# Optimization experiments

Measured on AMD Instinct MI355X. Metric: run time of the kernel, lower is better.

## Reference

```python
import jax, jax.numpy as jnp
import numpy as np

N_R, N_V, D, E_RR, L, G = 50000, 2000, 128, 800000, 3, 32


def setup_inputs() -> dict:
    key = jax.random.key(0)
    ks = jax.random.split(key, 10)
    x_real = jax.random.normal(ks[0], (N_R, D), dtype=jnp.float32)
    x_virtual = jax.random.normal(ks[1], (N_V, D), dtype=jnp.float32)
    # params: [num_layers, 3 relations (r_to_r, r_to_v, v_to_r), D, D]
    W_root = jax.random.normal(ks[2], (L, 3, D, D), dtype=jnp.float32) * 0.05
    W_nbr = jax.random.normal(ks[3], (L, 3, D, D), dtype=jnp.float32) * 0.05
    bias = jax.random.normal(ks[4], (L, 3, D), dtype=jnp.float32) * 0.05
    edge_rr = jax.random.randint(ks[5], (2, E_RR), 0, N_R)
    # one virtual-node edge per real node (hierarchical virtual nodes)
    src_rv = jnp.arange(N_R)
    dst_rv = jax.random.randint(ks[6], (N_R,), 0, N_V)
    edge_rv = jnp.stack([src_rv, dst_rv])          # real -> virtual
    edge_vr = jnp.stack([dst_rv, src_rv])          # virtual -> real
    batch_real = jnp.sort(jax.random.randint(ks[7], (N_R,), 0, G))
    return {
        "x_real": x_real, "x_virtual": x_virtual,
        "W_root": W_root, "W_nbr": W_nbr, "bias": bias,
        "edge_rr": edge_rr, "edge_rv": edge_rv, "edge_vr": edge_vr,
        "batch_real": batch_real,
    }


def _graph_conv(x_src, x_dst, src, dst, Wr, Wn, b, n_dst):
    # PyG GraphConv-style: root transform + sum-aggregated neighbor messages
    msg = jax.ops.segment_sum(x_src[src] @ Wn, dst, num_segments=n_dst)
    return x_dst @ Wr + msg + b


def _forward(x_real, x_virtual, W_root, W_nbr, bias, edge_rr, edge_rv, edge_vr, batch_real):
    x_r, x_v = x_real, x_virtual
    n_r, n_v = x_r.shape[0], x_v.shape[0]
    for l in range(W_root.shape[0]):
        # HeteroConv with aggr='sum': sum relation outputs per destination type
        c_rr = _graph_conv(x_r, x_r, edge_rr[0], edge_rr[1], W_root[l, 0], W_nbr[l, 0], bias[l, 0], n_r)
        c_vr = _graph_conv(x_v, x_r, edge_vr[0], edge_vr[1], W_root[l, 2], W_nbr[l, 2], bias[l, 2], n_r)
        c_rv = _graph_conv(x_r, x_v, edge_rv[0], edge_rv[1], W_root[l, 1], W_nbr[l, 1], bias[l, 1], n_v)
        # activation + dropout (eval mode -> identity)
        x_r = jax.nn.relu(c_rr + c_vr)
        x_v = jax.nn.relu(c_rv)
    # mean readout over real nodes per graph
    counts = jax.ops.segment_sum(jnp.ones((n_r,), x_r.dtype), batch_real, num_segments=G)
    graph_emb = jax.ops.segment_sum(x_r, batch_real, num_segments=G) / jnp.maximum(counts, 1.0)[:, None]
    return x_r, graph_emb


def reference(x_real, x_virtual, W_root, W_nbr, bias, edge_rr, edge_rv, edge_vr, batch_real):
    node_embedding, graph_embedding = _forward(
        x_real, x_virtual, W_root, W_nbr, bias, edge_rr, edge_rv, edge_vr, batch_real)
    return node_embedding, graph_embedding
```

## Files before the change

kernel.cpp:

```cpp
#include <hip/hip_runtime.h>
#include <hip/hip_bf16.h>

#define N_R   50000
#define N_V   2000
#define DIM   128
#define E_RR  800000
#define NLAY  3
#define NGR   32
#define RCHUNK 16

#define BUKD  128
#define NBUK  391
#define CHKE  2048
#define NCHK  391

typedef __attribute__((ext_vector_type(8))) short bf16x8;
typedef __attribute__((ext_vector_type(4))) float f32x4;
typedef __attribute__((ext_vector_type(2))) float f32x2;
typedef __attribute__((ext_vector_type(8))) unsigned char u8x8;

__device__ __forceinline__ ushort f2bf(float f) {
    unsigned u = __builtin_bit_cast(unsigned, f);
    unsigned r = (u + 0x7fffu + ((u >> 16) & 1u)) >> 16;
    return (ushort)r;
}
__device__ __forceinline__ float bf2f(ushort h) {
    unsigned u = ((unsigned)h) << 16;
    return __builtin_bit_cast(float, u);
}
__device__ __forceinline__ int lbound(const int* __restrict__ a, int n, int key) {
    int lo = 0, hi = n;
    while (lo < hi) { int mid = (lo + hi) >> 1; if (a[mid] < key) lo = mid + 1; else hi = mid; }
    return lo;
}

__device__ __forceinline__ void acc_u8row(
    unsigned w0, unsigned w1, float s,
    f32x2& a01, f32x2& a23, f32x2& a45, f32x2& a67)
{
    f32x2 sc = {s, s};
    a01 += sc * (f32x2){(float)(w0 & 0xffu), (float)((w0 >> 8) & 0xffu)};
    a23 += sc * (f32x2){(float)((w0 >> 16) & 0xffu), (float)(w0 >> 24)};
    a45 += sc * (f32x2){(float)(w1 & 0xffu), (float)((w1 >> 8) & 0xffu)};
    a67 += sc * (f32x2){(float)((w1 >> 16) & 0xffu), (float)(w1 >> 24)};
}

__global__ __launch_bounds__(256) void hist_kernel(
    const int* __restrict__ dst, int n, int* __restrict__ cnt)
{
    int i = blockIdx.x * 256 + threadIdx.x;
    if (i < n) atomicAdd(&cnt[dst[i]], 1);
}

__global__ __launch_bounds__(256) void scan_single_kernel(
    const int* __restrict__ cnt, int n, int nedges,
    int* __restrict__ rowptr, int* __restrict__ cursor)
{
    __shared__ int lds[256];
    __shared__ int carry;
    int t = threadIdx.x;
    if (t == 0) carry = 0;
    __syncthreads();
    for (int base = 0; base < n; base += 256) {
        int i = base + t;
        int v = (i < n) ? cnt[i] : 0;
        lds[t] = v;
        __syncthreads();
        #pragma unroll
        for (int off = 1; off < 256; off <<= 1) {
            int u = (t >= off) ? lds[t - off] : 0;
            __syncthreads();
            lds[t] += u;
            __syncthreads();
        }
        int excl = carry + lds[t] - v;
        if (i < n) {
            rowptr[i] = excl;
            if (cursor) cursor[i] = excl;
        }
        __syncthreads();
        if (t == 255) carry += lds[255];
        __syncthreads();
    }
    if (t == 0) rowptr[n] = nedges;
}

__global__ __launch_bounds__(256) void fill_kernel(
    const int* __restrict__ src, const int* __restrict__ dst, int n,
    int* __restrict__ cursor, int* __restrict__ col)
{
    int i = blockIdx.x * 256 + threadIdx.x;
    if (i < n) {
        int p = atomicAdd(&cursor[dst[i]], 1);
        col[p] = src[i];
    }
}

__global__ __launch_bounds__(256) void bkt_count_kernel(
    const int* __restrict__ dst, unsigned short* __restrict__ cnt2d)
{
    __shared__ int h[NBUK];
    int t = threadIdx.x, c = blockIdx.x;
    for (int i = t; i < NBUK; i += 256) h[i] = 0;
    __syncthreads();
    int e0 = c * CHKE, e1 = min(e0 + CHKE, E_RR);
    for (int e = e0 + t; e < e1; e += 256) atomicAdd(&h[dst[e] >> 7], 1);
    __syncthreads();
    for (int i = t; i < NBUK; i += 256)
        cnt2d[(size_t)c * NBUK + i] = (unsigned short)h[i];
}

__global__ __launch_bounds__(64) void bkt_prefix_kernel(
    const unsigned short* __restrict__ cnt2d,
    unsigned short* __restrict__ rel2d, int* __restrict__ tot)
{
    int b = blockIdx.x, lane = threadIdx.x;
    int base = 0;
    for (int c0 = 0; c0 < NCHK; c0 += 64) {
        int c = c0 + lane;
        int v = (c < NCHK) ? (int)cnt2d[(size_t)c * NBUK + b] : 0;
        int s = v;
        #pragma unroll
        for (int off = 1; off < 64; off <<= 1) {
            int u = __shfl_up(s, off);
            if (lane >= off) s += u;
        }
        if (c < NCHK) rel2d[(size_t)c * NBUK + b] = (unsigned short)(base + s - v);
        base += __shfl(s, 63);
    }
    if (lane == 0) tot[b] = base;
}

__global__ __launch_bounds__(256) void bkt_scatter_kernel(
    const int* __restrict__ src, const int* __restrict__ dst,
    const unsigned short* __restrict__ rel2d, const int* __restrict__ bstart,
    unsigned* __restrict__ ebuf)
{
    __shared__ int cur[NBUK];
    int t = threadIdx.x, c = blockIdx.x;
    for (int i = t; i < NBUK; i += 256)
        cur[i] = bstart[i] + (int)rel2d[(size_t)c * NBUK + i];
    __syncthreads();
    int e0 = c * CHKE, e1 = min(e0 + CHKE, E_RR);
    for (int e = e0 + t; e < e1; e += 256) {
        int d = dst[e];
        int p = atomicAdd(&cur[d >> 7], 1);
        ebuf[p] = ((unsigned)d << 16) | (unsigned)src[e];
    }
}

__global__ __launch_bounds__(256) void bkt_fine_kernel(
    const unsigned* __restrict__ ebuf, const int* __restrict__ bstart,
    int* __restrict__ rowptr, int* __restrict__ col)
{
    __shared__ int cnt[BUKD];
    __shared__ int sc[BUKD];
    __shared__ int cur[BUKD];
    int b = blockIdx.x, t = threadIdx.x;
    int s0 = bstart[b], s1 = bstart[b + 1];
    if (t < BUKD) cnt[t] = 0;
    __syncthreads();
    for (int e = s0 + t; e < s1; e += 256)
        atomicAdd(&cnt[(ebuf[e] >> 16) & (BUKD - 1)], 1);
    __syncthreads();
    if (t < BUKD) sc[t] = cnt[t];
    __syncthreads();
    #pragma unroll
    for (int off = 1; off < BUKD; off <<= 1) {
        int v = (t < BUKD && t >= off) ? sc[t - off] : 0;
        __syncthreads();
        if (t < BUKD) sc[t] += v;
        __syncthreads();
    }
    if (t < BUKD) {
        int ex = sc[t] - cnt[t];
        int d = b * BUKD + t;
        if (d < N_R) rowptr[d] = s0 + ex;
        cur[t] = ex;
    }
    if (b == NBUK - 1 && t == 0) rowptr[N_R] = E_RR;
    __syncthreads();
    for (int e = s0 + t; e < s1; e += 256) {
        unsigned pk = ebuf[e];
        int p = atomicAdd(&cur[(pk >> 16) & (BUKD - 1)], 1);
        col[s0 + p] = (int)(pk & 0xffffu);
    }
}

__global__ __launch_bounds__(256) void quant_input_kernel(
    const float* __restrict__ in, unsigned char* __restrict__ q,
    float2* __restrict__ meta)
{
    int w = (blockIdx.x * 256 + threadIdx.x) >> 6;
    int lane = threadIdx.x & 63;
    if (w >= N_R) return;
    float2 v = *(const float2*)(in + (size_t)w * DIM + lane * 2);
    float mn = fminf(v.x, v.y), mx = fmaxf(v.x, v.y);
    #pragma unroll
    for (int off = 1; off < 64; off <<= 1) {
        mn = fminf(mn, __shfl_xor(mn, off));
        mx = fmaxf(mx, __shfl_xor(mx, off));
    }
    float range = mx - mn;
    float inv = (range > 0.f) ? 255.f / range : 0.f;
    unsigned q0 = (unsigned)__float2int_rn((v.x - mn) * inv);
    unsigned q1 = (unsigned)__float2int_rn((v.y - mn) * inv);
    *(ushort*)(q + (size_t)w * DIM + lane * 2) = (ushort)(q0 | (q1 << 8));
    if (lane == 0) meta[w] = make_float2(range / 255.f, mn);
}

__global__ __launch_bounds__(256) void build_wt_kernel(
    const float* __restrict__ Wroot, const float* __restrict__ Wnbr,
    ushort* __restrict__ WT)
{
    int idx = blockIdx.x * 256 + threadIdx.x;
    if (idx >= NLAY * DIM * 2 * DIM) return;
    int k = idx & 255;
    int n = (idx >> 8) & 127;
    int l = idx >> 15;
    float v;
    if (k < DIM) {
        const float* base = Wroot + (size_t)l * 3 * DIM * DIM;
        v = base[(size_t)k * DIM + n] + base[(size_t)(2 * DIM + k) * DIM + n];
    } else {
        v = Wnbr[((size_t)l * 3 * DIM + (k - DIM)) * DIM + n];
    }
    WT[idx] = f2bf(v);
}

__global__ __launch_bounds__(256) void combine_b_kernel(
    const float* __restrict__ bias, float* __restrict__ bc)
{
    int idx = blockIdx.x * 256 + threadIdx.x;
    if (idx >= NLAY * DIM) return;
    int l = idx / DIM;
    int rest = idx - l * DIM;
    const float* base = bias + (size_t)l * 3 * DIM;
    bc[idx] = base[rest] + base[2 * DIM + rest];
}

__global__ __launch_bounds__(256) void vlayer_kernel(
    const int* __restrict__ rowptr, const int* __restrict__ col,
    const unsigned char* __restrict__ Xq, const float2* __restrict__ Xm,
    const float* __restrict__ xv,
    const float* __restrict__ Wn2, const float* __restrict__ Wr1,
    const float* __restrict__ Wn1, const float* __restrict__ b1,
    float* __restrict__ Tv, float* __restrict__ xv_next, int doNext)
{
    __shared__ float part[4 * DIM];
    __shared__ float arv_s[DIM];
    int v = blockIdx.x;
    int t = threadIdx.x;
    int wave = t >> 6, lane = t & 63;

    if (doNext) {
        int beg = rowptr[v], end = rowptr[v + 1];
        float a0 = 0.f, a1 = 0.f, msum = 0.f;
        for (int e = beg + wave; e < end; e += 4) {
            int c = col[e];
            float2 m = Xm[c];
            uchar2 u = *(const uchar2*)(Xq + (size_t)c * DIM + lane * 2);
            a0 += m.x * (float)u.x;
            a1 += m.x * (float)u.y;
            msum += m.y;
        }
        part[wave * DIM + lane * 2 + 0] = a0 + msum;
        part[wave * DIM + lane * 2 + 1] = a1 + msum;
        __syncthreads();
        if (t < DIM)
            arv_s[t] = part[t] + part[DIM + t] + part[2 * DIM + t] + part[3 * DIM + t];
        __syncthreads();
    }

    const float* arow = xv + (size_t)v * DIM;
    if (t < DIM) {
        float tacc = 0.f;
        #pragma unroll 8
        for (int k = 0; k < DIM; ++k)
            tacc += arow[k] * Wn2[(size_t)k * DIM + t];
        Tv[(size_t)v * DIM + t] = tacc;
    } else if (doNext) {
        int c = t - DIM;
        float nacc = 0.f;
        #pragma unroll 4
        for (int k = 0; k < DIM; ++k)
            nacc += arow[k] * Wr1[(size_t)k * DIM + c]
                  + arv_s[k] * Wn1[(size_t)k * DIM + c];
        xv_next[(size_t)v * DIM + c] = fmaxf(nacc + b1[c], 0.f);
    }
}

__global__ __launch_bounds__(128) void fused_layer_kernel(
    const int* __restrict__ rowptr, const int* __restrict__ col,
    const unsigned char* __restrict__ Xq, const float2* __restrict__ Xm,
    const ushort* __restrict__ WT,
    const float* __restrict__ Tv,  const int* __restrict__ vmap,
    const float* __restrict__ bias,
    float* __restrict__ outF,
    unsigned char* __restrict__ Xq_out, float2* __restrict__ Xm_out, int M)
{
    __shared__ ushort a2[16 * DIM];
    __shared__ float ost[16 * DIM];
    int t = threadIdx.x;

    int wave = t >> 6, lane = t & 63;
    int rlo = lane & 15, hi = lane >> 4;
    int row0 = blockIdx.x * 16;
    int arowc = min(row0 + rlo, M - 1);
    float2 am = Xm[arowc];
    bf16x8 afr[8];
    #pragma unroll
    for (int j = 0; j < 4; ++j) {
        u8x8 uv = *(const u8x8*)(Xq + (size_t)arowc * DIM + 32 * j + 8 * hi);
        bf16x8 f;
        #pragma unroll
        for (int q = 0; q < 8; ++q)
            f[q] = (short)f2bf(am.x * (float)uv[q] + am.y);
        afr[j] = f;
    }
    int vr[4];
    #pragma unroll
    for (int i = 0; i < 4; ++i)
        vr[i] = vmap[min(row0 + 4 * hi + i, M - 1)];

    int g = t >> 4;
    int li = t & 15;
    for (int rr = g; rr < 16; rr += 8) {
        int drow = min(row0 + rr, M - 1);
        int beg = rowptr[drow], end = rowptr[drow + 1];
        f32x2 a01 = {0.f, 0.f}, a23 = {0.f, 0.f};
        f32x2 a45 = {0.f, 0.f}, a67 = {0.f, 0.f};
        float msum = 0.f;
        int e = beg;
        for (; e + 3 < end; e += 4) {
            int c0 = col[e + 0], c1 = col[e + 1], c2 = col[e + 2], c3 = col[e + 3];
            float2 m0 = Xm[c0], m1 = Xm[c1], m2 = Xm[c2], m3 = Xm[c3];
            uint2 d0 = *(const uint2*)(Xq + (size_t)c0 * DIM + li * 8);
            uint2 d1 = *(const uint2*)(Xq + (size_t)c1 * DIM + li * 8);
            uint2 d2 = *(const uint2*)(Xq + (size_t)c2 * DIM + li * 8);
            uint2 d3 = *(const uint2*)(Xq + (size_t)c3 * DIM + li * 8);
            acc_u8row(d0.x, d0.y, m0.x, a01, a23, a45, a67);
            acc_u8row(d1.x, d1.y, m1.x, a01, a23, a45, a67);
            acc_u8row(d2.x, d2.y, m2.x, a01, a23, a45, a67);
            acc_u8row(d3.x, d3.y, m3.x, a01, a23, a45, a67);
            msum += (m0.y + m1.y) + (m2.y + m3.y);
        }
        for (; e < end; ++e) {
            int c0 = col[e];
            float2 m0 = Xm[c0];
            uint2 d0 = *(const uint2*)(Xq + (size_t)c0 * DIM + li * 8);
            acc_u8row(d0.x, d0.y, m0.x, a01, a23, a45, a67);
            msum += m0.y;
        }
        bf16x8 pk;
        pk[0] = (short)f2bf(a01.x + msum);
        pk[1] = (short)f2bf(a01.y + msum);
        pk[2] = (short)f2bf(a23.x + msum);
        pk[3] = (short)f2bf(a23.y + msum);
        pk[4] = (short)f2bf(a45.x + msum);
        pk[5] = (short)f2bf(a45.y + msum);
        pk[6] = (short)f2bf(a67.x + msum);
        pk[7] = (short)f2bf(a67.y + msum);
        int byte = rr * 256 + ((li * 16) ^ ((rr & 7) << 4));
        *(bf16x8*)((char*)a2 + byte) = pk;
    }
    __syncthreads();

    #pragma unroll
    for (int jj = 0; jj < 4; ++jj) {
        int byte = rlo * 256 + ((64 * jj + 16 * hi) ^ ((rlo & 7) << 4));
        afr[4 + jj] = *(const bf16x8*)((const char*)a2 + byte);
    }

    f32x4 acc[4];
    #pragma unroll
    for (int n = 0; n < 4; ++n) acc[n] = (f32x4){0.f, 0.f, 0.f, 0.f};

    #pragma unroll
    for (int n = 0; n < 4; ++n) {
        int nt = wave * 4 + n;
        const ushort* wrow = WT + (size_t)(nt * 16 + rlo) * (2 * DIM);
        #pragma unroll
        for (int j = 0; j < 8; ++j) {
            bf16x8 bfr = *(const bf16x8*)(wrow + 32 * j + 8 * hi);
            acc[n] = __builtin_amdgcn_mfma_f32_16x16x32_bf16(afr[j], bfr, acc[n], 0, 0, 0);
        }
    }

    if (outF) {
        #pragma unroll
        for (int n = 0; n < 4; ++n) {
            int ncol = (wave * 4 + n) * 16 + rlo;
            float bv = bias[ncol];
            #pragma unroll
            for (int i = 0; i < 4; ++i) {
                int orow = row0 + 4 * hi + i;
                if (orow >= M) continue;
                float v = acc[n][i] + bv + Tv[(size_t)vr[i] * DIM + ncol];
                outF[(size_t)orow * DIM + ncol] = fmaxf(v, 0.f);
            }
        }
    } else {
        #pragma unroll
        for (int n = 0; n < 4; ++n) {
            int ncol = (wave * 4 + n) * 16 + rlo;
            float bv = bias[ncol];
            #pragma unroll
            for (int i = 0; i < 4; ++i) {
                float v = acc[n][i] + bv + Tv[(size_t)vr[i] * DIM + ncol];
                ost[(4 * hi + i) * DIM + ncol] = fmaxf(v, 0.f);
            }
        }
        __syncthreads();
        for (int rr = g; rr < 16; rr += 8) {
            int orow = row0 + rr;
            float4 f0 = *(const float4*)(ost + rr * DIM + li * 8);
            float4 f1 = *(const float4*)(ost + rr * DIM + li * 8 + 4);
            float mn = fminf(fminf(fminf(f0.x, f0.y), fminf(f0.z, f0.w)),
                             fminf(fminf(f1.x, f1.y), fminf(f1.z, f1.w)));
            float mx = fmaxf(fmaxf(fmaxf(f0.x, f0.y), fmaxf(f0.z, f0.w)),
                             fmaxf(fmaxf(f1.x, f1.y), fmaxf(f1.z, f1.w)));
            #pragma unroll
            for (int off = 1; off < 16; off <<= 1) {
                mn = fminf(mn, __shfl_xor(mn, off, 16));
                mx = fmaxf(mx, __shfl_xor(mx, off, 16));
            }
            float range = mx - mn;
            float inv = (range > 0.f) ? 255.f / range : 0.f;
            if (orow < M) {
                u8x8 qv;
                qv[0] = (unsigned char)__float2int_rn((f0.x - mn) * inv);
                qv[1] = (unsigned char)__float2int_rn((f0.y - mn) * inv);
                qv[2] = (unsigned char)__float2int_rn((f0.z - mn) * inv);
                qv[3] = (unsigned char)__float2int_rn((f0.w - mn) * inv);
                qv[4] = (unsigned char)__float2int_rn((f1.x - mn) * inv);
                qv[5] = (unsigned char)__float2int_rn((f1.y - mn) * inv);
                qv[6] = (unsigned char)__float2int_rn((f1.z - mn) * inv);
                qv[7] = (unsigned char)__float2int_rn((f1.w - mn) * inv);
                *(u8x8*)(Xq_out + (size_t)orow * DIM + li * 8) = qv;
                if (li == 0) Xm_out[orow] = make_float2(range / 255.f, mn);
            }
        }
    }
}

__global__ __launch_bounds__(256) void readout_kernel(
    const float* __restrict__ xr, const int* __restrict__ batch,
    float* __restrict__ gsum, int nrows)
{
    __shared__ float lds[256 * 4];
    int g = blockIdx.x / RCHUNK;
    int chunk = blockIdx.x % RCHUNK;
    int lo = lbound(batch, nrows, g);
    int hi = lbound(batch, nrows, g + 1);
    int len = hi - lo;
    if (len == 0) return;
    int per = (len + RCHUNK - 1) / RCHUNK;
    int r0 = lo + chunk * per;
    int r1 = min(r0 + per, hi);

    int t = threadIdx.x;
    int c4 = (t & 31) << 2;
    int rsub = t >> 5;

    float4 acc = make_float4(0.f, 0.f, 0.f, 0.f);
    for (int r = r0 + rsub; r < r1; r += 8) {
        float4 v = *(const float4*)(xr + (size_t)r * DIM + c4);
        acc.x += v.x; acc.y += v.y; acc.z += v.z; acc.w += v.w;
    }
    *(float4*)(lds + t * 4) = acc;
    __syncthreads();
    if (rsub == 0) {
        float4 s = make_float4(0.f, 0.f, 0.f, 0.f);
        #pragma unroll
        for (int j = 0; j < 8; ++j) {
            float4 v = *(const float4*)(lds + (j * 32 + t) * 4);
            s.x += v.x; s.y += v.y; s.z += v.z; s.w += v.w;
        }
        atomicAdd(&gsum[(size_t)g * DIM + c4 + 0], s.x);
        atomicAdd(&gsum[(size_t)g * DIM + c4 + 1], s.y);
        atomicAdd(&gsum[(size_t)g * DIM + c4 + 2], s.z);
        atomicAdd(&gsum[(size_t)g * DIM + c4 + 3], s.w);
    }
}

__global__ __launch_bounds__(256) void finalize_kernel(
    const float* __restrict__ gsum, const int* __restrict__ batch,
    float* __restrict__ out, int nrows)
{
    int idx = blockIdx.x * 256 + threadIdx.x;
    if (idx >= NGR * DIM) return;
    int g = idx >> 7;
    int lo = lbound(batch, nrows, g);
    int hi = lbound(batch, nrows, g + 1);
    float c = fmaxf((float)(hi - lo), 1.f);
    out[idx] = gsum[idx] / c;
}

extern "C" void kernel_launch(void* const* d_in, const int* in_sizes, int n_in,
                              void* d_out, int out_size, void* d_ws, size_t ws_size,
                              hipStream_t stream)
{
    const float* x_real    = (const float*)d_in[0];
    const float* x_virtual = (const float*)d_in[1];
    const float* W_root    = (const float*)d_in[2];
    const float* W_nbr     = (const float*)d_in[3];
    const float* bias      = (const float*)d_in[4];
    const int*   edge_rr   = (const int*)d_in[5];
    const int*   edge_rv   = (const int*)d_in[6];
    const int*   edge_vr   = (const int*)d_in[7];
    const int*   batch     = (const int*)d_in[8];

    float* out = (float*)d_out;

    float2* meta0 = (float2*)d_ws;
    float2* meta1 = meta0 + N_R;
    float2* meta2 = meta1 + N_R;
    float*  Tv    = (float*)(meta2 + N_R);
    float*  xv_a  = Tv   + (size_t)N_V * DIM;
    float*  xv_b  = xv_a + (size_t)N_V * DIM;
    float*  bc    = xv_b + (size_t)N_V * DIM;
    float*  gsum  = bc   + (size_t)NLAY * DIM;
    ushort* WT    = (ushort*)(gsum + NGR * DIM);
    int* iws       = (int*)(WT + (size_t)NLAY * DIM * 2 * DIM);
    int* rowptr_rr = iws;
    int* col_rr    = rowptr_rr + N_R + 1;
    int* cnt_v     = col_rr + E_RR;
    int* rowptr_rv = cnt_v + N_V;
    int* cursor_rv = rowptr_rv + N_V + 1;
    int* col_rv    = cursor_rv + N_V;
    int* tot       = col_rv + N_R;
    int* bstart    = tot + NBUK;
    unsigned short* cnt2d = (unsigned short*)(bstart + NBUK + 1);
    unsigned short* rel2d = cnt2d + (size_t)NCHK * NBUK;
    unsigned* ebuf = (unsigned*)(rel2d + (size_t)NCHK * NBUK + 2);
    unsigned char* Q0 = (unsigned char*)(ebuf + E_RR);
    unsigned char* Q1 = Q0 + (size_t)N_R * DIM;
    unsigned char* Q2 = Q1 + (size_t)N_R * DIM;

    const int* rr_src = edge_rr;
    const int* rr_dst = edge_rr + E_RR;
    const int* rv_src = edge_rv;
    const int* rv_dst = edge_rv + N_R;

    bkt_count_kernel<<<NCHK, 256, 0, stream>>>(rr_dst, cnt2d);
    bkt_prefix_kernel<<<NBUK, 64, 0, stream>>>(cnt2d, rel2d, tot);
    scan_single_kernel<<<1, 256, 0, stream>>>(tot, NBUK, E_RR, bstart, nullptr);
    bkt_scatter_kernel<<<NCHK, 256, 0, stream>>>(rr_src, rr_dst, rel2d, bstart, ebuf);
    bkt_fine_kernel<<<NBUK, 256, 0, stream>>>(ebuf, bstart, rowptr_rr, col_rr);

    hipMemsetAsync(cnt_v, 0, (size_t)N_V * sizeof(int), stream);
    hist_kernel<<<(N_R + 255) / 256, 256, 0, stream>>>(rv_dst, N_R, cnt_v);
    scan_single_kernel<<<1, 256, 0, stream>>>(cnt_v, N_V, N_R, rowptr_rv, cursor_rv);
    fill_kernel<<<(N_R + 255) / 256, 256, 0, stream>>>(rv_src, rv_dst, N_R, cursor_rv, col_rv);

    build_wt_kernel<<<(NLAY * DIM * 2 * DIM + 255) / 256, 256, 0, stream>>>(W_root, W_nbr, WT);
    combine_b_kernel<<<(NLAY * DIM + 255) / 256, 256, 0, stream>>>(bias, bc);
    quant_input_kernel<<<(N_R * 64 + 255) / 256, 256, 0, stream>>>(x_real, Q0, meta0);

    unsigned char* Qcur = Q0;  float2* Mcur = meta0;
    const float* cur_xv = x_virtual;

    for (int l = 0; l < NLAY; ++l) {
        const float* Wn1 = W_nbr + ((size_t)l * 3 + 1) * DIM * DIM;
        const float* Wn2 = W_nbr + ((size_t)l * 3 + 2) * DIM * DIM;
        const float* Wr1 = W_root + ((size_t)l * 3 + 1) * DIM * DIM;
        const float* b1  = bias + ((size_t)l * 3 + 1) * DIM;

        int doNext = (l < NLAY - 1);
        float* xv_out = (l & 1) ? xv_b : xv_a;

        vlayer_kernel<<<N_V, 256, 0, stream>>>(
            rowptr_rv, col_rv, Qcur, Mcur, cur_xv,
            Wn2, Wr1, Wn1, b1, Tv, xv_out, doNext);

        unsigned char* Qnext = (l == 0) ? Q1 : Q2;
        float2*        Mnext = (l == 0) ? meta1 : meta2;
        float* outF = (l == NLAY - 1) ? out : nullptr;
        fused_layer_kernel<<<(N_R + 15) / 16, 128, 0, stream>>>(
            rowptr_rr, col_rr, Qcur, Mcur, WT + (size_t)l * DIM * 2 * DIM,
            Tv, edge_vr, bc + (size_t)l * DIM,
            outF, outF ? nullptr : Qnext, outF ? nullptr : Mnext, N_R);

        if (doNext) { cur_xv = xv_out; Qcur = Qnext; Mcur = Mnext; }
    }

    hipMemsetAsync(gsum, 0, (size_t)NGR * DIM * sizeof(float), stream);
    readout_kernel<<<NGR * RCHUNK, 256, 0, stream>>>(out, batch, gsum, N_R);
    finalize_kernel<<<(NGR * DIM + 255) / 256, 256, 0, stream>>>(
        gsum, batch, out + (size_t)N_R * DIM, N_R);
}
```

Measured before the change: 330.2 us.

## Split quantized features into column planes and gather in separate half passes

Result: slower. 365.1 us (+10.6%).

```diff
diff --git a/kernel.cpp b/kernel.cpp
--- a/kernel.cpp
+++ b/kernel.cpp
@@ -18,6 +18,8 @@
 typedef __attribute__((ext_vector_type(4))) float f32x4;
 typedef __attribute__((ext_vector_type(2))) float f32x2;
 typedef __attribute__((ext_vector_type(8))) unsigned char u8x8;
+
+#define NR64 ((size_t)N_R * 64)
 
 __device__ __forceinline__ ushort f2bf(float f) {
     unsigned u = __builtin_bit_cast(unsigned, f);
@@ -205,7 +207,10 @@
     float inv = (range > 0.f) ? 255.f / range : 0.f;
     unsigned q0 = (unsigned)__float2int_rn((v.x - mn) * inv);
     unsigned q1 = (unsigned)__float2int_rn((v.y - mn) * inv);
-    *(ushort*)(q + (size_t)w * DIM + lane * 2) = (ushort)(q0 | (q1 << 8));
+    int plane = lane >> 5;
+    int off2 = (lane * 2) & 63;
+    *(ushort*)(q + (size_t)plane * NR64 + (size_t)w * 64 + off2)
+        = (ushort)(q0 | (q1 << 8));
     if (lane == 0) meta[w] = make_float2(range / 255.f, mn);
 }
 
@@ -239,6 +244,52 @@
     bc[idx] = base[rest] + base[2 * DIM + rest];
 }
 
+__global__ __launch_bounds__(256) void gather_half_kernel(
+    const int* __restrict__ rowptr, const int* __restrict__ col,
+    const unsigned char* __restrict__ XH,
+    const float2* __restrict__ Xm,
+    ushort* __restrict__ A2, int half, int nrows)
+{
+    int g = (blockIdx.x * 256 + threadIdx.x) >> 3;
+    int li = threadIdx.x & 7;
+    if (g >= nrows) return;
+    int beg = rowptr[g], end = rowptr[g + 1];
+    f32x2 a01 = {0.f, 0.f}, a23 = {0.f, 0.f};
+    f32x2 a45 = {0.f, 0.f}, a67 = {0.f, 0.f};
+    float msum = 0.f;
+    int e = beg;
+    for (; e + 3 < end; e += 4) {
+        int c0 = col[e + 0], c1 = col[e + 1], c2 = col[e + 2], c3 = col[e + 3];
+        float2 m0 = Xm[c0], m1 = Xm[c1], m2 = Xm[c2], m3 = Xm[c3];
+        uint2 d0 = *(const uint2*)(XH + (size_t)c0 * 64 + li * 8);
+        uint2 d1 = *(const uint2*)(XH + (size_t)c1 * 64 + li * 8);
+        uint2 d2 = *(const uint2*)(XH + (size_t)c2 * 64 + li * 8);
+        uint2 d3 = *(const uint2*)(XH + (size_t)c3 * 64 + li * 8);
+        acc_u8row(d0.x, d0.y, m0.x, a01, a23, a45, a67);
+        acc_u8row(d1.x, d1.y, m1.x, a01, a23, a45, a67);
+        acc_u8row(d2.x, d2.y, m2.x, a01, a23, a45, a67);
+        acc_u8row(d3.x, d3.y, m3.x, a01, a23, a45, a67);
+        msum += (m0.y + m1.y) + (m2.y + m3.y);
+    }
+    for (; e < end; ++e) {
+        int c0 = col[e];
+        float2 m0 = Xm[c0];
+        uint2 d0 = *(const uint2*)(XH + (size_t)c0 * 64 + li * 8);
+        acc_u8row(d0.x, d0.y, m0.x, a01, a23, a45, a67);
+        msum += m0.y;
+    }
+    bf16x8 pk;
+    pk[0] = (short)f2bf(a01.x + msum);
+    pk[1] = (short)f2bf(a01.y + msum);
+    pk[2] = (short)f2bf(a23.x + msum);
+    pk[3] = (short)f2bf(a23.y + msum);
+    pk[4] = (short)f2bf(a45.x + msum);
+    pk[5] = (short)f2bf(a45.y + msum);
+    pk[6] = (short)f2bf(a67.x + msum);
+    pk[7] = (short)f2bf(a67.y + msum);
+    *(bf16x8*)(A2 + (size_t)g * DIM + half * 64 + li * 8) = pk;
+}
+
 __global__ __launch_bounds__(256) void vlayer_kernel(
     const int* __restrict__ rowptr, const int* __restrict__ col,
     const unsigned char* __restrict__ Xq, const float2* __restrict__ Xm,
@@ -254,12 +305,14 @@
     int wave = t >> 6, lane = t & 63;
 
     if (doNext) {
+        const unsigned char* XP = Xq + (size_t)(lane >> 5) * NR64;
+        int joff = (lane * 2) & 63;
         int beg = rowptr[v], end = rowptr[v + 1];
         float a0 = 0.f, a1 = 0.f, msum = 0.f;
         for (int e = beg + wave; e < end; e += 4) {
             int c = col[e];
             float2 m = Xm[c];
-            uchar2 u = *(const uchar2*)(Xq + (size_t)c * DIM + lane * 2);
+            uchar2 u = *(const uchar2*)(XP + (size_t)c * 64 + joff);
             a0 += m.x * (float)u.x;
             a1 += m.x * (float)u.y;
             msum += m.y;
@@ -290,16 +343,14 @@
     }
 }
 
-__global__ __launch_bounds__(128) void fused_layer_kernel(
-    const int* __restrict__ rowptr, const int* __restrict__ col,
+__global__ __launch_bounds__(128) void mfma_layer_kernel(
     const unsigned char* __restrict__ Xq, const float2* __restrict__ Xm,
-    const ushort* __restrict__ WT,
+    const ushort* __restrict__ A2, const ushort* __restrict__ WT,
     const float* __restrict__ Tv,  const int* __restrict__ vmap,
     const float* __restrict__ bias,
     float* __restrict__ outF,
     unsigned char* __restrict__ Xq_out, float2* __restrict__ Xm_out, int M)
 {
-    __shared__ ushort a2[16 * DIM];
     __shared__ float ost[16 * DIM];
     int t = threadIdx.x;
 
@@ -311,66 +362,23 @@
     bf16x8 afr[8];
     #pragma unroll
     for (int j = 0; j < 4; ++j) {
-        u8x8 uv = *(const u8x8*)(Xq + (size_t)arowc * DIM + 32 * j + 8 * hi);
+        int k = 32 * j + 8 * hi;
+        const unsigned char* src = Xq + (size_t)(k >> 6) * NR64
+                                 + (size_t)arowc * 64 + (k & 63);
+        u8x8 uv = *(const u8x8*)src;
         bf16x8 f;
         #pragma unroll
         for (int q = 0; q < 8; ++q)
             f[q] = (short)f2bf(am.x * (float)uv[q] + am.y);
         afr[j] = f;
     }
+    #pragma unroll
+    for (int jj = 0; jj < 4; ++jj)
+        afr[4 + jj] = *(const bf16x8*)(A2 + (size_t)arowc * DIM + 32 * jj + 8 * hi);
     int vr[4];
     #pragma unroll
     for (int i = 0; i < 4; ++i)
         vr[i] = vmap[min(row0 + 4 * hi + i, M - 1)];
-
-    int g = t >> 4;
-    int li = t & 15;
-    for (int rr = g; rr < 16; rr += 8) {
-        int drow = min(row0 + rr, M - 1);
-        int beg = rowptr[drow], end = rowptr[drow + 1];
-        f32x2 a01 = {0.f, 0.f}, a23 = {0.f, 0.f};
-        f32x2 a45 = {0.f, 0.f}, a67 = {0.f, 0.f};
-        float msum = 0.f;
-        int e = beg;
-        for (; e + 3 < end; e += 4) {
-            int c0 = col[e + 0], c1 = col[e + 1], c2 = col[e + 2], c3 = col[e + 3];
-            float2 m0 = Xm[c0], m1 = Xm[c1], m2 = Xm[c2], m3 = Xm[c3];
-            uint2 d0 = *(const uint2*)(Xq + (size_t)c0 * DIM + li * 8);
-            uint2 d1 = *(const uint2*)(Xq + (size_t)c1 * DIM + li * 8);
-            uint2 d2 = *(const uint2*)(Xq + (size_t)c2 * DIM + li * 8);
-            uint2 d3 = *(const uint2*)(Xq + (size_t)c3 * DIM + li * 8);
-            acc_u8row(d0.x, d0.y, m0.x, a01, a23, a45, a67);
-            acc_u8row(d1.x, d1.y, m1.x, a01, a23, a45, a67);
-            acc_u8row(d2.x, d2.y, m2.x, a01, a23, a45, a67);
-            acc_u8row(d3.x, d3.y, m3.x, a01, a23, a45, a67);
-            msum += (m0.y + m1.y) + (m2.y + m3.y);
-        }
-        for (; e < end; ++e) {
-            int c0 = col[e];
-            float2 m0 = Xm[c0];
-            uint2 d0 = *(const uint2*)(Xq + (size_t)c0 * DIM + li * 8);
-            acc_u8row(d0.x, d0.y, m0.x, a01, a23, a45, a67);
-            msum += m0.y;
-        }
-        bf16x8 pk;
-        pk[0] = (short)f2bf(a01.x + msum);
-        pk[1] = (short)f2bf(a01.y + msum);
-        pk[2] = (short)f2bf(a23.x + msum);
-        pk[3] = (short)f2bf(a23.y + msum);
-        pk[4] = (short)f2bf(a45.x + msum);
-        pk[5] = (short)f2bf(a45.y + msum);
-        pk[6] = (short)f2bf(a67.x + msum);
-        pk[7] = (short)f2bf(a67.y + msum);
-        int byte = rr * 256 + ((li * 16) ^ ((rr & 7) << 4));
-        *(bf16x8*)((char*)a2 + byte) = pk;
-    }
-    __syncthreads();
-
-    #pragma unroll
-    for (int jj = 0; jj < 4; ++jj) {
-        int byte = rlo * 256 + ((64 * jj + 16 * hi) ^ ((rlo & 7) << 4));
-        afr[4 + jj] = *(const bf16x8*)((const char*)a2 + byte);
-    }
 
     f32x4 acc[4];
     #pragma unroll
@@ -412,6 +420,8 @@
             }
         }
         __syncthreads();
+        int g = t >> 4;
+        int li = t & 15;
         for (int rr = g; rr < 16; rr += 8) {
             int orow = row0 + rr;
             float4 f0 = *(const float4*)(ost + rr * DIM + li * 8);
@@ -437,7 +447,8 @@
                 qv[5] = (unsigned char)__float2int_rn((f1.y - mn) * inv);
                 qv[6] = (unsigned char)__float2int_rn((f1.z - mn) * inv);
                 qv[7] = (unsigned char)__float2int_rn((f1.w - mn) * inv);
-                *(u8x8*)(Xq_out + (size_t)orow * DIM + li * 8) = qv;
+                *(u8x8*)(Xq_out + (size_t)(li >> 3) * NR64
+                         + (size_t)orow * 64 + ((li * 8) & 63)) = qv;
                 if (li == 0) Xm_out[orow] = make_float2(range / 255.f, mn);
             }
         }
@@ -521,7 +532,8 @@
     float*  xv_b  = xv_a + (size_t)N_V * DIM;
     float*  bc    = xv_b + (size_t)N_V * DIM;
     float*  gsum  = bc   + (size_t)NLAY * DIM;
-    ushort* WT    = (ushort*)(gsum + NGR * DIM);
+    ushort* A2buf = (ushort*)(gsum + NGR * DIM);
+    ushort* WT    = A2buf + (size_t)N_R * DIM;
     int* iws       = (int*)(WT + (size_t)NLAY * DIM * 2 * DIM);
     int* rowptr_rr = iws;
     int* col_rr    = rowptr_rr + N_R + 1;
@@ -561,6 +573,8 @@
     unsigned char* Qcur = Q0;  float2* Mcur = meta0;
     const float* cur_xv = x_virtual;
 
+    const int gatherGrid = (N_R * 8 + 255) / 256;
+
     for (int l = 0; l < NLAY; ++l) {
         const float* Wn1 = W_nbr + ((size_t)l * 3 + 1) * DIM * DIM;
         const float* Wn2 = W_nbr + ((size_t)l * 3 + 2) * DIM * DIM;
@@ -574,11 +588,16 @@
             rowptr_rv, col_rv, Qcur, Mcur, cur_xv,
             Wn2, Wr1, Wn1, b1, Tv, xv_out, doNext);
 
+        gather_half_kernel<<<gatherGrid, 256, 0, stream>>>(
+            rowptr_rr, col_rr, Qcur,        Mcur, A2buf, 0, N_R);
+        gather_half_kernel<<<gatherGrid, 256, 0, stream>>>(
+            rowptr_rr, col_rr, Qcur + NR64, Mcur, A2buf, 1, N_R);
+
         unsigned char* Qnext = (l == 0) ? Q1 : Q2;
         float2*        Mnext = (l == 0) ? meta1 : meta2;
         float* outF = (l == NLAY - 1) ? out : nullptr;
-        fused_layer_kernel<<<(N_R + 15) / 16, 128, 0, stream>>>(
-            rowptr_rr, col_rr, Qcur, Mcur, WT + (size_t)l * DIM * 2 * DIM,
+        mfma_layer_kernel<<<(N_R + 15) / 16, 128, 0, stream>>>(
+            Qcur, Mcur, A2buf, WT + (size_t)l * DIM * 2 * DIM,
             Tv, edge_vr, bc + (size_t)l * DIM,
             outF, outF ? nullptr : Qnext, outF ? nullptr : Mnext, N_R);
 
```

## Double threads per block in fused layer kernel, splitting gather rows in halves

Applied to the files above, without the earlier changes.

Result: faster. 319.8 us (-3.2%).

```diff
diff --git a/kernel.cpp b/kernel.cpp
--- a/kernel.cpp
+++ b/kernel.cpp
@@ -290,7 +290,7 @@
     }
 }
 
-__global__ __launch_bounds__(128) void fused_layer_kernel(
+__global__ __launch_bounds__(256) void fused_layer_kernel(
     const int* __restrict__ rowptr, const int* __restrict__ col,
     const unsigned char* __restrict__ Xq, const float2* __restrict__ Xm,
     const ushort* __restrict__ WT,
@@ -323,11 +323,14 @@
     for (int i = 0; i < 4; ++i)
         vr[i] = vmap[min(row0 + 4 * hi + i, M - 1)];
 
-    int g = t >> 4;
-    int li = t & 15;
-    for (int rr = g; rr < 16; rr += 8) {
-        int drow = min(row0 + rr, M - 1);
+    {
+        int g = t >> 3;
+        int li = t & 7;
+        int row = g >> 1;
+        int half = g & 1;
+        int drow = min(row0 + row, M - 1);
         int beg = rowptr[drow], end = rowptr[drow + 1];
+        const unsigned char* XH = Xq + half * 64 + li * 8;
         f32x2 a01 = {0.f, 0.f}, a23 = {0.f, 0.f};
         f32x2 a45 = {0.f, 0.f}, a67 = {0.f, 0.f};
         float msum = 0.f;
@@ -335,10 +338,10 @@
         for (; e + 3 < end; e += 4) {
             int c0 = col[e + 0], c1 = col[e + 1], c2 = col[e + 2], c3 = col[e + 3];
             float2 m0 = Xm[c0], m1 = Xm[c1], m2 = Xm[c2], m3 = Xm[c3];
-            uint2 d0 = *(const uint2*)(Xq + (size_t)c0 * DIM + li * 8);
-            uint2 d1 = *(const uint2*)(Xq + (size_t)c1 * DIM + li * 8);
-            uint2 d2 = *(const uint2*)(Xq + (size_t)c2 * DIM + li * 8);
-            uint2 d3 = *(const uint2*)(Xq + (size_t)c3 * DIM + li * 8);
+            uint2 d0 = *(const uint2*)(XH + (size_t)c0 * DIM);
+            uint2 d1 = *(const uint2*)(XH + (size_t)c1 * DIM);
+            uint2 d2 = *(const uint2*)(XH + (size_t)c2 * DIM);
+            uint2 d3 = *(const uint2*)(XH + (size_t)c3 * DIM);
             acc_u8row(d0.x, d0.y, m0.x, a01, a23, a45, a67);
             acc_u8row(d1.x, d1.y, m1.x, a01, a23, a45, a67);
             acc_u8row(d2.x, d2.y, m2.x, a01, a23, a45, a67);
@@ -348,7 +351,7 @@
         for (; e < end; ++e) {
             int c0 = col[e];
             float2 m0 = Xm[c0];
-            uint2 d0 = *(const uint2*)(Xq + (size_t)c0 * DIM + li * 8);
+            uint2 d0 = *(const uint2*)(XH + (size_t)c0 * DIM);
             acc_u8row(d0.x, d0.y, m0.x, a01, a23, a45, a67);
             msum += m0.y;
         }
@@ -361,7 +364,7 @@
         pk[5] = (short)f2bf(a45.y + msum);
         pk[6] = (short)f2bf(a67.x + msum);
         pk[7] = (short)f2bf(a67.y + msum);
-        int byte = rr * 256 + ((li * 16) ^ ((rr & 7) << 4));
+        int byte = row * 256 + ((half * 128 + li * 16) ^ ((row & 7) << 4));
         *(bf16x8*)((char*)a2 + byte) = pk;
     }
     __syncthreads();
@@ -372,13 +375,13 @@
         afr[4 + jj] = *(const bf16x8*)((const char*)a2 + byte);
     }
 
-    f32x4 acc[4];
-    #pragma unroll
-    for (int n = 0; n < 4; ++n) acc[n] = (f32x4){0.f, 0.f, 0.f, 0.f};
-
-    #pragma unroll
-    for (int n = 0; n < 4; ++n) {
-        int nt = wave * 4 + n;
+    f32x4 acc[2];
+    #pragma unroll
+    for (int n = 0; n < 2; ++n) acc[n] = (f32x4){0.f, 0.f, 0.f, 0.f};
+
+    #pragma unroll
+    for (int n = 0; n < 2; ++n) {
+        int nt = wave * 2 + n;
         const ushort* wrow = WT + (size_t)(nt * 16 + rlo) * (2 * DIM);
         #pragma unroll
         for (int j = 0; j < 8; ++j) {
@@ -389,8 +392,8 @@
 
     if (outF) {
         #pragma unroll
-        for (int n = 0; n < 4; ++n) {
-            int ncol = (wave * 4 + n) * 16 + rlo;
+        for (int n = 0; n < 2; ++n) {
+            int ncol = (wave * 2 + n) * 16 + rlo;
             float bv = bias[ncol];
             #pragma unroll
             for (int i = 0; i < 4; ++i) {
@@ -402,8 +405,8 @@
         }
     } else {
         #pragma unroll
-        for (int n = 0; n < 4; ++n) {
-            int ncol = (wave * 4 + n) * 16 + rlo;
+        for (int n = 0; n < 2; ++n) {
+            int ncol = (wave * 2 + n) * 16 + rlo;
             float bv = bias[ncol];
             #pragma unroll
             for (int i = 0; i < 4; ++i) {
@@ -412,34 +415,34 @@
             }
         }
         __syncthreads();
-        for (int rr = g; rr < 16; rr += 8) {
-            int orow = row0 + rr;
-            float4 f0 = *(const float4*)(ost + rr * DIM + li * 8);
-            float4 f1 = *(const float4*)(ost + rr * DIM + li * 8 + 4);
-            float mn = fminf(fminf(fminf(f0.x, f0.y), fminf(f0.z, f0.w)),
-                             fminf(fminf(f1.x, f1.y), fminf(f1.z, f1.w)));
-            float mx = fmaxf(fmaxf(fmaxf(f0.x, f0.y), fmaxf(f0.z, f0.w)),
-                             fmaxf(fmaxf(f1.x, f1.y), fmaxf(f1.z, f1.w)));
-            #pragma unroll
-            for (int off = 1; off < 16; off <<= 1) {
-                mn = fminf(mn, __shfl_xor(mn, off, 16));
-                mx = fmaxf(mx, __shfl_xor(mx, off, 16));
-            }
-            float range = mx - mn;
-            float inv = (range > 0.f) ? 255.f / range : 0.f;
-            if (orow < M) {
-                u8x8 qv;
-                qv[0] = (unsigned char)__float2int_rn((f0.x - mn) * inv);
-                qv[1] = (unsigned char)__float2int_rn((f0.y - mn) * inv);
-                qv[2] = (unsigned char)__float2int_rn((f0.z - mn) * inv);
-                qv[3] = (unsigned char)__float2int_rn((f0.w - mn) * inv);
-                qv[4] = (unsigned char)__float2int_rn((f1.x - mn) * inv);
-                qv[5] = (unsigned char)__float2int_rn((f1.y - mn) * inv);
-                qv[6] = (unsigned char)__float2int_rn((f1.z - mn) * inv);
-                qv[7] = (unsigned char)__float2int_rn((f1.w - mn) * inv);
-                *(u8x8*)(Xq_out + (size_t)orow * DIM + li * 8) = qv;
-                if (li == 0) Xm_out[orow] = make_float2(range / 255.f, mn);
-            }
+        int g16 = t >> 4;
+        int li16 = t & 15;
+        int orow = row0 + g16;
+        float4 f0 = *(const float4*)(ost + g16 * DIM + li16 * 8);
+        float4 f1 = *(const float4*)(ost + g16 * DIM + li16 * 8 + 4);
+        float mn = fminf(fminf(fminf(f0.x, f0.y), fminf(f0.z, f0.w)),
+                         fminf(fminf(f1.x, f1.y), fminf(f1.z, f1.w)));
+        float mx = fmaxf(fmaxf(fmaxf(f0.x, f0.y), fmaxf(f0.z, f0.w)),
+                         fmaxf(fmaxf(f1.x, f1.y), fmaxf(f1.z, f1.w)));
+        #pragma unroll
+        for (int off = 1; off < 16; off <<= 1) {
+            mn = fminf(mn, __shfl_xor(mn, off, 16));
+            mx = fmaxf(mx, __shfl_xor(mx, off, 16));
+        }
+        float range = mx - mn;
+        float inv = (range > 0.f) ? 255.f / range : 0.f;
+        if (orow < M) {
+            u8x8 qv;
+            qv[0] = (unsigned char)__float2int_rn((f0.x - mn) * inv);
+            qv[1] = (unsigned char)__float2int_rn((f0.y - mn) * inv);
+            qv[2] = (unsigned char)__float2int_rn((f0.z - mn) * inv);
+            qv[3] = (unsigned char)__float2int_rn((f0.w - mn) * inv);
+            qv[4] = (unsigned char)__float2int_rn((f1.x - mn) * inv);
+            qv[5] = (unsigned char)__float2int_rn((f1.y - mn) * inv);
+            qv[6] = (unsigned char)__float2int_rn((f1.z - mn) * inv);
+            qv[7] = (unsigned char)__float2int_rn((f1.w - mn) * inv);
+            *(u8x8*)(Xq_out + (size_t)orow * DIM + li16 * 8) = qv;
+            if (li16 == 0) Xm_out[orow] = make_float2(range / 255.f, mn);
         }
     }
 }
@@ -577,7 +580,7 @@
         unsigned char* Qnext = (l == 0) ? Q1 : Q2;
         float2*        Mnext = (l == 0) ? meta1 : meta2;
         float* outF = (l == NLAY - 1) ? out : nullptr;
-        fused_layer_kernel<<<(N_R + 15) / 16, 128, 0, stream>>>(
+        fused_layer_kernel<<<(N_R + 15) / 16, 256, 0, stream>>>(
             rowptr_rr, col_rr, Qcur, Mcur, WT + (size_t)l * DIM * 2 * DIM,
             Tv, edge_vr, bc + (size_t)l * DIM,
             outF, outF ? nullptr : Qnext, outF ? nullptr : Mnext, N_R);
```
